# Kernel tuning notes

Measured on AMD Instinct MI355X. Metric: run time of the kernel, lower is better.

The kernel has to match this reference:

```python
import jax, jax.numpy as jnp
import numpy as np

N = 131072          # source points
M = 65536           # sampled (query) points
NN = 32             # max_nr_neighbors
K = 15              # num_kernel_points
IN_F = 64
OUT_F = 128
MAP_SIZE = 40.0
SUB_DIST = 0.5      # subsampling_dist * subsampling_factor (meters)
KERNEL_RADIUS = max(1.5, 2.0 * SUB_DIST) / MAP_SIZE          # 0.0375
KP_EXTENT = KERNEL_RADIUS / (K ** (1.0 / 3.0) - 1.0) * 1.5
NEG_SLOPE = 0.01    # nn.LeakyReLU default


def setup_inputs() -> dict:
    rng = np.random.RandomState(0)
    points = rng.rand(N, 3).astype(np.float32)

    # ---- gridSampling (faithful numpy port of the torch code) ----
    resolution = SUB_DIST / MAP_SIZE
    grid = np.floor(points / resolution)
    center = (grid + 0.5) * resolution
    dist = ((points - center) ** 2).sum(1)
    dist = dist / dist.max() * 0.7
    v_size = np.ceil(1.0 / resolution)
    grid_idx = grid[:, 0] + grid[:, 1] * v_size + grid[:, 2] * v_size * v_size
    grid_d = grid_idx + dist
    order = np.argsort(grid_d, kind='stable')
    gi_sorted = grid_idx[order]
    first = np.ones(N, bool)
    first[1:] = gi_sorted[1:] != gi_sorted[:-1]
    sample_idx = order[first]  # closest-to-voxel-center point per voxel
    if sample_idx.shape[0] < M:
        sample_idx = np.tile(sample_idx, int(np.ceil(M / sample_idx.shape[0])))
    sample_idx = np.sort(sample_idx[:M])

    # ---- radius search (stand-in for octree.radiusSearchIndices) ----
    # candidates = window in voxel-sorted order, filtered by true euclidean radius,
    # nearest-first, padded with shadow index N (standard KPConv padding).
    pos_in_sorted = np.empty(N, np.int64)
    pos_in_sorted[order] = np.arange(N)
    qpos = pos_in_sorted[sample_idx]
    offs = np.arange(-48, 48)
    cand_pos = np.clip(qpos[:, None] + offs[None, :], 0, N - 1)
    cand_idx = order[cand_pos]                                  # [M,96]
    d2 = ((points[cand_idx] - points[sample_idx][:, None, :]) ** 2).sum(-1)
    valid = d2 <= KERNEL_RADIUS ** 2
    d2w = np.where(valid, d2, np.inf)
    sel = np.argsort(d2w, axis=1)[:, :NN]
    nbr = np.take_along_axis(cand_idx, sel, 1)
    nbr_ok = np.take_along_axis(valid, sel, 1)
    neighbors_index = np.where(nbr_ok, nbr, N).astype(np.int32)  # [M,NN]

    # ---- kernel point dispositions (rigid KPConv buffer) ----
    kp_dir = rng.randn(K, 3).astype(np.float32)
    kp_dir /= np.linalg.norm(kp_dir, axis=1, keepdims=True) + 1e-9
    kernel_points = kp_dir * (rng.rand(K, 1).astype(np.float32) ** (1.0 / 3.0)) * KERNEL_RADIUS

    key = jax.random.key(0)
    ks = jax.random.split(key, 6)
    def lin(k, i, o):
        return (jax.random.normal(k, (i, o), jnp.float32) / np.sqrt(i)).astype(jnp.float32)

    return {
        'points': jnp.asarray(points),
        'features': jax.random.normal(ks[0], (N, IN_F), jnp.float32),
        'W_pre': lin(ks[1], IN_F, OUT_F),
        'b_pre': jnp.zeros((OUT_F,), jnp.float32),
        'kernel_points': jnp.asarray(kernel_points),
        'kp_weights': jax.random.normal(ks[2], (K, OUT_F, OUT_F), jnp.float32) / np.sqrt(K * OUT_F),
        'W_post': lin(ks[3], OUT_F, OUT_F),
        'b_post': jnp.zeros((OUT_F,), jnp.float32),
        'W_sc': lin(ks[4], IN_F, OUT_F),
        'b_sc': jnp.zeros((OUT_F,), jnp.float32),
        'sample_idx': jnp.asarray(sample_idx, jnp.int32),
        'neighbors_index': jnp.asarray(neighbors_index),
    }


def _leaky(x):
    return jnp.where(x >= 0, x, NEG_SLOPE * x)


def reference(points, features, W_pre, b_pre, kernel_points, kp_weights,
              W_post, b_post, W_sc, b_sc, sample_idx, neighbors_index):
    # preactivation: Linear + LeakyReLU (batchnorm=False)
    feats = _leaky(features @ W_pre + b_pre)                       # [N, OUT_F]

    # shadow padding: far point + zero feature row at index N
    s_pts = jnp.concatenate([points, jnp.full((1, 3), 1e6, points.dtype)], 0)
    x_pad = jnp.concatenate([feats, jnp.zeros((1, OUT_F), feats.dtype)], 0)

    # rigid KPConv: gather -> distance influence -> weight -> aggregate
    q_pts = points[sample_idx]                                     # [M,3]
    neighb = s_pts[neighbors_index] - q_pts[:, None, :]            # [M,NN,3]
    sq_d = jnp.sum((neighb[:, :, None, :] - kernel_points[None, None]) ** 2, -1)  # [M,NN,K]
    all_w = jnp.maximum(1.0 - jnp.sqrt(sq_d) / KP_EXTENT, 0.0)     # linear influence
    nx = x_pad[neighbors_index]                                    # [M,NN,OUT_F]
    wfeat = jnp.einsum('mnk,mnc->mkc', all_w, nx)                  # [M,K,OUT_F]
    conv = jnp.einsum('mkc,kco->mo', wfeat, kp_weights)            # [M,OUT_F]

    # post layer: LeakyReLU then Linear (batchnorm=False, relu=True)
    post = _leaky(conv) @ W_post + b_post

    # shortcut on sampled input features (in_fdim != out_fdim -> Linear)
    sc = features[sample_idx] @ W_sc + b_sc
    return _leaky(sc + post)                                       # [M,OUT_F]
```

## Files before the change

kernel.cpp:

```cpp
#include <hip/hip_runtime.h>
#include <cmath>

#define NPTS 131072
#define MTOT 65536
#define NNB  32
#define KKP  15
#define INF  64
#define OUTF 128
#define KCDIM 1920
#define WROWB 1920

#define META_OFF  61440
#define LDS_TOTAL 77824
#define A2_OFF 0
#define A3_OFF 8192

typedef __attribute__((ext_vector_type(8))) __bf16 bf16x8;
typedef __attribute__((ext_vector_type(8))) unsigned short u16x8;
typedef __attribute__((ext_vector_type(4))) float f32x4;
typedef unsigned int u32;
typedef __attribute__((ext_vector_type(4))) u32 u32x4;

__device__ __forceinline__ u32 f2bf(float f){
  u32 u = __builtin_bit_cast(u32, f);
  return (u + 0x7fffu + ((u>>16)&1u)) >> 16;
}
__device__ __forceinline__ float leaky(float v){ return v >= 0.f ? v : 0.01f*v; }

__global__ __launch_bounds__(256) void k_cvt_67723(
    const float* __restrict__ kpw, const float* __restrict__ wpost,
    const float* __restrict__ wsc, const float* __restrict__ wpre,
    unsigned short* __restrict__ bpack, unsigned short* __restrict__ wpostT,
    unsigned short* __restrict__ wscT, unsigned short* __restrict__ wpreT)
{
  int tid = blockIdx.x * 256 + threadIdx.x;
  if (tid < KCDIM * OUTF) {
    int kc = tid >> 7, o = tid & 127;
    int kk = kc >> 7, c = kc & 127;
    int h = c >> 6, cl = c & 63;
    int s = kk*2 + (cl >> 5);
    int rem = cl & 31, lg = rem >> 3, j = rem & 7;
    int ot = o >> 4, lr = o & 15;
    bpack[(size_t)((h*30 + s)*8 + ot)*512 + lr*32 + lg*8 + j] =
        (unsigned short)f2bf(kpw[(size_t)kc * OUTF + o]);
    return;
  }
  int t2 = tid - KCDIM * OUTF;
  if (t2 < OUTF * OUTF) {
    int o = t2 / OUTF, i = t2 % OUTF;
    wpostT[t2] = (unsigned short)f2bf(wpost[i * OUTF + o]);
    return;
  }
  int t3 = t2 - OUTF * OUTF;
  if (t3 < OUTF * INF) {
    int o = t3 / INF, c = t3 % INF;
    wscT[t3] = (unsigned short)f2bf(wsc[c * OUTF + o]);
    return;
  }
  int t4 = t3 - OUTF * INF;
  if (t4 < OUTF * INF) {
    int o = t4 / INF, c = t4 % INF;
    wpreT[t4] = (unsigned short)f2bf(wpre[c * OUTF + o]);
  }
}

__global__ __launch_bounds__(256) void k_pre_67723(
    const float* __restrict__ feat, const unsigned short* __restrict__ wpreT,
    const float* __restrict__ bp, unsigned short* __restrict__ featbf)
{
  const int w = threadIdx.x >> 6, l = threadIdx.x & 63, lr = l & 15, lg = l >> 4;
  const int m0 = blockIdx.x * 128 + w * 32;
  f32x4 acc[2][8];
#pragma unroll
  for (int ot = 0; ot < 8; ot++) {
    float bv = bp[ot*16 + lr];
    f32x4 s = {bv, bv, bv, bv};
    acc[0][ot] = s; acc[1][ot] = s;
  }
  bf16x8 af[2][2];
#pragma unroll
  for (int mi = 0; mi < 2; mi++)
#pragma unroll
  for (int ks = 0; ks < 2; ks++) {
    const float* src = feat + (size_t)(m0 + mi*16 + lr) * INF + ks*32 + lg*8;
    float4 f0 = *(const float4*)src, f1 = *(const float4*)(src + 4);
    u16x8 p;
    p[0]=f2bf(f0.x); p[1]=f2bf(f0.y); p[2]=f2bf(f0.z); p[3]=f2bf(f0.w);
    p[4]=f2bf(f1.x); p[5]=f2bf(f1.y); p[6]=f2bf(f1.z); p[7]=f2bf(f1.w);
    af[mi][ks] = __builtin_bit_cast(bf16x8, p);
  }
#pragma unroll
  for (int ks = 0; ks < 2; ks++)
#pragma unroll
  for (int ot = 0; ot < 8; ot++) {
    bf16x8 b = *(const bf16x8*)(wpreT + (size_t)(ot*16 + lr) * INF + ks*32 + lg*8);
    acc[0][ot] = __builtin_amdgcn_mfma_f32_16x16x32_bf16(af[0][ks], b, acc[0][ot], 0,0,0);
    acc[1][ot] = __builtin_amdgcn_mfma_f32_16x16x32_bf16(af[1][ks], b, acc[1][ot], 0,0,0);
  }
#pragma unroll
  for (int mi = 0; mi < 2; mi++)
#pragma unroll
  for (int ot = 0; ot < 8; ot++)
#pragma unroll
  for (int r = 0; r < 4; r++) {
    int m = m0 + mi*16 + lg*4 + r;
    featbf[(size_t)m * OUTF + ot*16 + lr] = (unsigned short)f2bf(leaky(acc[mi][ot][r]));
  }
}

__global__ __launch_bounds__(512, 4) void k_fused_67723(
    const float* __restrict__ points, const float* __restrict__ features,
    const float* __restrict__ kp, const float* __restrict__ bpost,
    const float* __restrict__ bsc, const int* __restrict__ sample_idx,
    const int* __restrict__ nbr, const unsigned short* __restrict__ featbf,
    const unsigned short* __restrict__ bpack, const unsigned short* __restrict__ wpostT,
    const unsigned short* __restrict__ wscT, float* __restrict__ out,
    float inv_ext, int nwg)
{
  extern __shared__ char smem[];
  float4* meta = (float4*)(smem + META_OFF);
  const int t = threadIdx.x, l = t & 63, w = t >> 6, lr = l & 15, lg = l >> 4;
  const int bid = blockIdx.x;
  const int swb = (bid & 7) * (nwg >> 3) + (bid >> 3);
  const int m0 = swb * 32;

  for (int e = t; e < 1024; e += 512) {
    int s = e >> 5, n = e & 31;
    int gm = m0 + s;
    int sidx = sample_idx[gm];
    int ni = nbr[(size_t)gm * NNB + n];
    bool valid = ni < NPTS;
    int nic = valid ? ni : 0;
    float qx = points[sidx*3], qy = points[sidx*3+1], qz = points[sidx*3+2];
    float dx = points[nic*3] - qx, dy = points[nic*3+1] - qy, dz = points[nic*3+2] - qz;
    if (!valid) dx = 1e9f;
    meta[s*32 + n] = make_float4(dx, dy, dz, __int_as_float(nic * (OUTF*2)));
  }
  __syncthreads();

  const bool kvalid = lr < KKP;
  const int kk2 = kvalid ? lr : 0;
  const float kx = kp[kk2*3], ky = kp[kk2*3+1], kz = kp[kk2*3+2];
  const char* fb = (const char*)featbf;
  const f32x4 zero = {0,0,0,0};

  f32x4 acc[2] = {{0,0,0,0},{0,0,0,0}};
  const int convswz = (lr & 7) << 4;
  const char* arow0 = smem + lr * WROWB;
  const char* arow1 = smem + (lr + 16) * WROWB;

#pragma unroll
  for (int h = 0; h < 2; h++) {
    if (h) __syncthreads();

    for (int i = 0; i < 4; i++) {
      const int s = w*4 + i;
      uint2 dj[8];
      u32 apk[4];
      float wvp = 0.f;
#pragma unroll
      for (int j = 0; j < 8; j++) {
        float4 mje = meta[s*32 + lg*8 + j];
        u32 off = __builtin_bit_cast(u32, mje.w);
        dj[j] = *(const uint2*)(fb + off + h*128 + lr*8);
        float ex = mje.x - kx, ey = mje.y - ky, ez = mje.z - kz;
        float d = sqrtf(ex*ex + ey*ey + ez*ez);
        float wv = kvalid ? fmaxf(1.f - d * inv_ext, 0.f) : 0.f;
        if (j & 1) apk[j>>1] = f2bf(wvp) | (f2bf(wv) << 16);
        else       wvp = wv;
      }
      u32x4 av = {apk[0], apk[1], apk[2], apk[3]};
      bf16x8 afr = __builtin_bit_cast(bf16x8, av);

      f32x4 D[4];
#pragma unroll
      for (int q = 0; q < 4; q++) {
        u32 b[4];
#pragma unroll
        for (int u = 0; u < 4; u++) {
          u32 w0 = (q < 2) ? dj[2*u].x   : dj[2*u].y;
          u32 w1 = (q < 2) ? dj[2*u+1].x : dj[2*u+1].y;
          b[u] = __builtin_amdgcn_perm(w1, w0, (q & 1) ? 0x07060302u : 0x05040100u);
        }
        u32x4 bv = {b[0], b[1], b[2], b[3]};
        D[q] = __builtin_amdgcn_mfma_f32_16x16x32_bf16(
                   afr, __builtin_bit_cast(bf16x8, bv), zero, 0,0,0);
      }
      char* wrow = smem + s * WROWB;
      const int sswz = (s & 7) << 4;
#pragma unroll
      for (int r = 0; r < 4; r++) {
        int kr = lg*4 + r;
        if (kr < KKP) {
          uint2 pv;
          pv.x = f2bf(D[0][r]) | (f2bf(D[1][r]) << 16);
          pv.y = f2bf(D[2][r]) | (f2bf(D[3][r]) << 16);
          *(uint2*)(wrow + ((kr*128 + lr*8) ^ sswz)) = pv;
        }
      }
    }
    __syncthreads();

    const char* bb = (const char*)bpack + (size_t)(h*240 + w) * 1024 + lr*64 + lg*16;
#pragma unroll 6
    for (int s = 0; s < 30; s++) {
      int aoff = (s*64 + lg*16) ^ convswz;
      bf16x8 af0 = *(const bf16x8*)(arow0 + aoff);
      bf16x8 af1 = *(const bf16x8*)(arow1 + aoff);
      bf16x8 bfr = *(const bf16x8*)(bb + s*8192);
      acc[0] = __builtin_amdgcn_mfma_f32_16x16x32_bf16(af0, bfr, acc[0], 0,0,0);
      acc[1] = __builtin_amdgcn_mfma_f32_16x16x32_bf16(af1, bfr, acc[1], 0,0,0);
    }
  }
  __syncthreads();

  char* a2 = smem + A2_OFF;
  char* a3 = smem + A3_OFF;
#pragma unroll
  for (int mi = 0; mi < 2; mi++)
#pragma unroll
  for (int r = 0; r < 4; r++) {
    int m = mi*16 + lg*4 + r;
    int o = w*16 + lr;
    *(unsigned short*)(a2 + m*256 + ((o*2) ^ ((m & 15) << 4))) =
        (unsigned short)f2bf(leaky(acc[mi][r]));
  }
  if (t < 256) {
    int r = t >> 3, seg = t & 7;
    int sidx = sample_idx[m0 + r];
    const float* src = features + (size_t)sidx * INF + seg*8;
    float4 f0 = *(const float4*)src, f1 = *(const float4*)(src + 4);
    uint4 pv = make_uint4(f2bf(f0.x) | (f2bf(f0.y) << 16),
                          f2bf(f0.z) | (f2bf(f0.w) << 16),
                          f2bf(f1.x) | (f2bf(f1.y) << 16),
                          f2bf(f1.z) | (f2bf(f1.w) << 16));
    *(uint4*)(a3 + r*128 + ((seg*16) ^ ((r & 7) << 4))) = pv;
  }
  __syncthreads();

  const int mt = w & 1, oq = w >> 1;
  const int mrow = mt*16 + lr;
  f32x4 d[2];
#pragma unroll
  for (int ot = 0; ot < 2; ot++) {
    float bv = bpost[oq*32 + ot*16 + lr] + bsc[oq*32 + ot*16 + lr];
    d[ot] = (f32x4){bv, bv, bv, bv};
  }
#pragma unroll
  for (int ks = 0; ks < 4; ks++) {
    bf16x8 af = *(const bf16x8*)(a2 + mrow*256 + ((ks*64 + lg*16) ^ ((mrow & 15) << 4)));
#pragma unroll
    for (int ot = 0; ot < 2; ot++) {
      bf16x8 b = *(const bf16x8*)(wpostT + (size_t)(oq*32 + ot*16 + lr) * OUTF + ks*32 + lg*8);
      d[ot] = __builtin_amdgcn_mfma_f32_16x16x32_bf16(af, b, d[ot], 0,0,0);
    }
  }
#pragma unroll
  for (int ks = 0; ks < 2; ks++) {
    bf16x8 af = *(const bf16x8*)(a3 + mrow*128 + ((ks*64 + lg*16) ^ ((mrow & 7) << 4)));
#pragma unroll
    for (int ot = 0; ot < 2; ot++) {
      bf16x8 b = *(const bf16x8*)(wscT + (size_t)(oq*32 + ot*16 + lr) * INF + ks*32 + lg*8);
      d[ot] = __builtin_amdgcn_mfma_f32_16x16x32_bf16(af, b, d[ot], 0,0,0);
    }
  }
#pragma unroll
  for (int ot = 0; ot < 2; ot++)
#pragma unroll
  for (int r = 0; r < 4; r++) {
    int m = mt*16 + lg*4 + r;
    int o = oq*32 + ot*16 + lr;
    out[(size_t)(m0 + m) * OUTF + o] = leaky(d[ot][r]);
  }
}

extern "C" void kernel_launch(void* const* d_in, const int* in_sizes, int n_in,
                              void* d_out, int out_size, void* d_ws, size_t ws_size,
                              hipStream_t stream)
{
  const float* points   = (const float*)d_in[0];
  const float* features = (const float*)d_in[1];
  const float* W_pre    = (const float*)d_in[2];
  const float* b_pre    = (const float*)d_in[3];
  const float* kpts     = (const float*)d_in[4];
  const float* kpw      = (const float*)d_in[5];
  const float* W_post   = (const float*)d_in[6];
  const float* b_post   = (const float*)d_in[7];
  const float* W_sc     = (const float*)d_in[8];
  const float* b_sc     = (const float*)d_in[9];
  const int* sample_idx = (const int*)d_in[10];
  const int* nbr        = (const int*)d_in[11];
  float* out = (float*)d_out;

  char* ws = (char*)d_ws;
  unsigned short* featbf = (unsigned short*)ws;
  unsigned short* bpack  = (unsigned short*)(ws + 33554432);
  unsigned short* wpostT = (unsigned short*)(ws + 34045952);
  unsigned short* wscT   = (unsigned short*)(ws + 34078720);
  unsigned short* wpreT  = (unsigned short*)(ws + 34095104);

  double ext = (1.5 / 40.0) / (pow(15.0, 1.0 / 3.0) - 1.0) * 1.5;
  float inv_ext = (float)(1.0 / ext);

  (void)hipFuncSetAttribute((const void*)k_fused_67723,
                            hipFuncAttributeMaxDynamicSharedMemorySize, LDS_TOTAL);

  const int nwg = MTOT / 32;
  k_cvt_67723<<<1088, 256, 0, stream>>>(kpw, W_post, W_sc, W_pre, bpack, wpostT, wscT, wpreT);
  k_pre_67723<<<1024, 256, 0, stream>>>(features, wpreT, b_pre, featbf);
  k_fused_67723<<<nwg, 512, LDS_TOTAL, stream>>>(points, features, kpts, b_post, b_sc,
                                                 sample_idx, nbr, featbf, bpack, wpostT,
                                                 wscT, out, inv_ext, nwg);
}
```

Measured before the change: 173.4 us.

## Make fused blocks loop over four M-tiles with conv weights held in registers

Measured after the change: 644.9 us. 272% more time.

```diff
diff --git a/kernel.cpp b/kernel.cpp
--- a/kernel.cpp
+++ b/kernel.cpp
@@ -115,162 +115,173 @@
     const int* __restrict__ nbr, const unsigned short* __restrict__ featbf,
     const unsigned short* __restrict__ bpack, const unsigned short* __restrict__ wpostT,
     const unsigned short* __restrict__ wscT, float* __restrict__ out,
-    float inv_ext, int nwg)
+    float inv_ext)
 {
   extern __shared__ char smem[];
   float4* meta = (float4*)(smem + META_OFF);
   const int t = threadIdx.x, l = t & 63, w = t >> 6, lr = l & 15, lg = l >> 4;
   const int bid = blockIdx.x;
-  const int swb = (bid & 7) * (nwg >> 3) + (bid >> 3);
-  const int m0 = swb * 32;
-
-  for (int e = t; e < 1024; e += 512) {
-    int s = e >> 5, n = e & 31;
-    int gm = m0 + s;
-    int sidx = sample_idx[gm];
-    int ni = nbr[(size_t)gm * NNB + n];
-    bool valid = ni < NPTS;
-    int nic = valid ? ni : 0;
-    float qx = points[sidx*3], qy = points[sidx*3+1], qz = points[sidx*3+2];
-    float dx = points[nic*3] - qx, dy = points[nic*3+1] - qy, dz = points[nic*3+2] - qz;
-    if (!valid) dx = 1e9f;
-    meta[s*32 + n] = make_float4(dx, dy, dz, __int_as_float(nic * (OUTF*2)));
-  }
-  __syncthreads();
+  const int swb = (bid & 7) * 64 + (bid >> 3);
+  const int mblk = swb * 128;
+
+  bf16x8 Breg[60];
+  {
+    const char* bp = (const char*)bpack + (size_t)w * 1024 + lr*64 + lg*16;
+#pragma unroll
+    for (int f = 0; f < 60; f++)
+      Breg[f] = *(const bf16x8*)(bp + (size_t)f * 8192);
+  }
 
   const bool kvalid = lr < KKP;
   const int kk2 = kvalid ? lr : 0;
   const float kx = kp[kk2*3], ky = kp[kk2*3+1], kz = kp[kk2*3+2];
   const char* fb = (const char*)featbf;
   const f32x4 zero = {0,0,0,0};
-
-  f32x4 acc[2] = {{0,0,0,0},{0,0,0,0}};
   const int convswz = (lr & 7) << 4;
   const char* arow0 = smem + lr * WROWB;
   const char* arow1 = smem + (lr + 16) * WROWB;
-
-#pragma unroll
-  for (int h = 0; h < 2; h++) {
-    if (h) __syncthreads();
-
-    for (int i = 0; i < 4; i++) {
-      const int s = w*4 + i;
-      uint2 dj[8];
-      u32 apk[4];
-      float wvp = 0.f;
-#pragma unroll
-      for (int j = 0; j < 8; j++) {
-        float4 mje = meta[s*32 + lg*8 + j];
-        u32 off = __builtin_bit_cast(u32, mje.w);
-        dj[j] = *(const uint2*)(fb + off + h*128 + lr*8);
-        float ex = mje.x - kx, ey = mje.y - ky, ez = mje.z - kz;
-        float d = sqrtf(ex*ex + ey*ey + ez*ez);
-        float wv = kvalid ? fmaxf(1.f - d * inv_ext, 0.f) : 0.f;
-        if (j & 1) apk[j>>1] = f2bf(wvp) | (f2bf(wv) << 16);
-        else       wvp = wv;
-      }
-      u32x4 av = {apk[0], apk[1], apk[2], apk[3]};
-      bf16x8 afr = __builtin_bit_cast(bf16x8, av);
-
-      f32x4 D[4];
-#pragma unroll
-      for (int q = 0; q < 4; q++) {
-        u32 b[4];
-#pragma unroll
-        for (int u = 0; u < 4; u++) {
-          u32 w0 = (q < 2) ? dj[2*u].x   : dj[2*u].y;
-          u32 w1 = (q < 2) ? dj[2*u+1].x : dj[2*u+1].y;
-          b[u] = __builtin_amdgcn_perm(w1, w0, (q & 1) ? 0x07060302u : 0x05040100u);
+  const int mt_e = w & 1, oq_e = w >> 1;
+  const int mrow = mt_e*16 + lr;
+
+  for (int tile = 0; tile < 4; tile++) {
+    const int m0 = mblk + tile * 32;
+    __syncthreads();
+
+    for (int e = t; e < 1024; e += 512) {
+      int s = e >> 5, n = e & 31;
+      int gm = m0 + s;
+      int sidx = sample_idx[gm];
+      int ni = nbr[(size_t)gm * NNB + n];
+      bool valid = ni < NPTS;
+      int nic = valid ? ni : 0;
+      float qx = points[sidx*3], qy = points[sidx*3+1], qz = points[sidx*3+2];
+      float dx = points[nic*3] - qx, dy = points[nic*3+1] - qy, dz = points[nic*3+2] - qz;
+      if (!valid) dx = 1e9f;
+      meta[s*32 + n] = make_float4(dx, dy, dz, __int_as_float(nic * (OUTF*2)));
+    }
+    __syncthreads();
+
+    f32x4 acc[2] = {{0,0,0,0},{0,0,0,0}};
+
+#pragma unroll
+    for (int h = 0; h < 2; h++) {
+      if (h) __syncthreads();
+
+      for (int i = 0; i < 4; i++) {
+        const int s = w*4 + i;
+        uint2 dj[8];
+        u32 apk[4];
+        float wvp = 0.f;
+#pragma unroll
+        for (int j = 0; j < 8; j++) {
+          float4 mje = meta[s*32 + lg*8 + j];
+          u32 off = __builtin_bit_cast(u32, mje.w);
+          dj[j] = *(const uint2*)(fb + off + h*128 + lr*8);
+          float ex = mje.x - kx, ey = mje.y - ky, ez = mje.z - kz;
+          float d = sqrtf(ex*ex + ey*ey + ez*ez);
+          float wv = kvalid ? fmaxf(1.f - d * inv_ext, 0.f) : 0.f;
+          if (j & 1) apk[j>>1] = f2bf(wvp) | (f2bf(wv) << 16);
+          else       wvp = wv;
         }
-        u32x4 bv = {b[0], b[1], b[2], b[3]};
-        D[q] = __builtin_amdgcn_mfma_f32_16x16x32_bf16(
-                   afr, __builtin_bit_cast(bf16x8, bv), zero, 0,0,0);
-      }
-      char* wrow = smem + s * WROWB;
-      const int sswz = (s & 7) << 4;
-#pragma unroll
-      for (int r = 0; r < 4; r++) {
-        int kr = lg*4 + r;
-        if (kr < KKP) {
-          uint2 pv;
-          pv.x = f2bf(D[0][r]) | (f2bf(D[1][r]) << 16);
-          pv.y = f2bf(D[2][r]) | (f2bf(D[3][r]) << 16);
-          *(uint2*)(wrow + ((kr*128 + lr*8) ^ sswz)) = pv;
+        u32x4 av = {apk[0], apk[1], apk[2], apk[3]};
+        bf16x8 afr = __builtin_bit_cast(bf16x8, av);
+
+        f32x4 D[4];
+#pragma unroll
+        for (int q = 0; q < 4; q++) {
+          u32 b[4];
+#pragma unroll
+          for (int u = 0; u < 4; u++) {
+            u32 w0 = (q < 2) ? dj[2*u].x   : dj[2*u].y;
+            u32 w1 = (q < 2) ? dj[2*u+1].x : dj[2*u+1].y;
+            b[u] = __builtin_amdgcn_perm(w1, w0, (q & 1) ? 0x07060302u : 0x05040100u);
+          }
+          u32x4 bv = {b[0], b[1], b[2], b[3]};
+          D[q] = __builtin_amdgcn_mfma_f32_16x16x32_bf16(
+                     afr, __builtin_bit_cast(bf16x8, bv), zero, 0,0,0);
+        }
+        char* wrow = smem + s * WROWB;
+        const int sswz = (s & 7) << 4;
+#pragma unroll
+        for (int r = 0; r < 4; r++) {
+          int kr = lg*4 + r;
+          if (kr < KKP) {
+            uint2 pv;
+            pv.x = f2bf(D[0][r]) | (f2bf(D[1][r]) << 16);
+            pv.y = f2bf(D[2][r]) | (f2bf(D[3][r]) << 16);
+            *(uint2*)(wrow + ((kr*128 + lr*8) ^ sswz)) = pv;
+          }
         }
       }
+      __syncthreads();
+
+#pragma unroll
+      for (int s = 0; s < 30; s++) {
+        int aoff = (s*64 + lg*16) ^ convswz;
+        bf16x8 af0 = *(const bf16x8*)(arow0 + aoff);
+        bf16x8 af1 = *(const bf16x8*)(arow1 + aoff);
+        acc[0] = __builtin_amdgcn_mfma_f32_16x16x32_bf16(af0, Breg[h*30+s], acc[0], 0,0,0);
+        acc[1] = __builtin_amdgcn_mfma_f32_16x16x32_bf16(af1, Breg[h*30+s], acc[1], 0,0,0);
+      }
     }
     __syncthreads();
 
-    const char* bb = (const char*)bpack + (size_t)(h*240 + w) * 1024 + lr*64 + lg*16;
-#pragma unroll 6
-    for (int s = 0; s < 30; s++) {
-      int aoff = (s*64 + lg*16) ^ convswz;
-      bf16x8 af0 = *(const bf16x8*)(arow0 + aoff);
-      bf16x8 af1 = *(const bf16x8*)(arow1 + aoff);
-      bf16x8 bfr = *(const bf16x8*)(bb + s*8192);
-      acc[0] = __builtin_amdgcn_mfma_f32_16x16x32_bf16(af0, bfr, acc[0], 0,0,0);
-      acc[1] = __builtin_amdgcn_mfma_f32_16x16x32_bf16(af1, bfr, acc[1], 0,0,0);
-    }
-  }
-  __syncthreads();
-
-  char* a2 = smem + A2_OFF;
-  char* a3 = smem + A3_OFF;
-#pragma unroll
-  for (int mi = 0; mi < 2; mi++)
-#pragma unroll
-  for (int r = 0; r < 4; r++) {
-    int m = mi*16 + lg*4 + r;
-    int o = w*16 + lr;
-    *(unsigned short*)(a2 + m*256 + ((o*2) ^ ((m & 15) << 4))) =
-        (unsigned short)f2bf(leaky(acc[mi][r]));
-  }
-  if (t < 256) {
-    int r = t >> 3, seg = t & 7;
-    int sidx = sample_idx[m0 + r];
-    const float* src = features + (size_t)sidx * INF + seg*8;
-    float4 f0 = *(const float4*)src, f1 = *(const float4*)(src + 4);
-    uint4 pv = make_uint4(f2bf(f0.x) | (f2bf(f0.y) << 16),
-                          f2bf(f0.z) | (f2bf(f0.w) << 16),
-                          f2bf(f1.x) | (f2bf(f1.y) << 16),
-                          f2bf(f1.z) | (f2bf(f1.w) << 16));
-    *(uint4*)(a3 + r*128 + ((seg*16) ^ ((r & 7) << 4))) = pv;
-  }
-  __syncthreads();
-
-  const int mt = w & 1, oq = w >> 1;
-  const int mrow = mt*16 + lr;
-  f32x4 d[2];
-#pragma unroll
-  for (int ot = 0; ot < 2; ot++) {
-    float bv = bpost[oq*32 + ot*16 + lr] + bsc[oq*32 + ot*16 + lr];
-    d[ot] = (f32x4){bv, bv, bv, bv};
-  }
-#pragma unroll
-  for (int ks = 0; ks < 4; ks++) {
-    bf16x8 af = *(const bf16x8*)(a2 + mrow*256 + ((ks*64 + lg*16) ^ ((mrow & 15) << 4)));
+    char* a2 = smem + A2_OFF;
+    char* a3 = smem + A3_OFF;
+#pragma unroll
+    for (int mi = 0; mi < 2; mi++)
+#pragma unroll
+    for (int r = 0; r < 4; r++) {
+      int m = mi*16 + lg*4 + r;
+      int o = w*16 + lr;
+      *(unsigned short*)(a2 + m*256 + ((o*2) ^ ((m & 15) << 4))) =
+          (unsigned short)f2bf(leaky(acc[mi][r]));
+    }
+    if (t < 256) {
+      int r = t >> 3, seg = t & 7;
+      int sidx = sample_idx[m0 + r];
+      const float* src = features + (size_t)sidx * INF + seg*8;
+      float4 f0 = *(const float4*)src, f1 = *(const float4*)(src + 4);
+      uint4 pv = make_uint4(f2bf(f0.x) | (f2bf(f0.y) << 16),
+                            f2bf(f0.z) | (f2bf(f0.w) << 16),
+                            f2bf(f1.x) | (f2bf(f1.y) << 16),
+                            f2bf(f1.z) | (f2bf(f1.w) << 16));
+      *(uint4*)(a3 + r*128 + ((seg*16) ^ ((r & 7) << 4))) = pv;
+    }
+    __syncthreads();
+
+    f32x4 d[2];
 #pragma unroll
     for (int ot = 0; ot < 2; ot++) {
-      bf16x8 b = *(const bf16x8*)(wpostT + (size_t)(oq*32 + ot*16 + lr) * OUTF + ks*32 + lg*8);
-      d[ot] = __builtin_amdgcn_mfma_f32_16x16x32_bf16(af, b, d[ot], 0,0,0);
-    }
-  }
-#pragma unroll
-  for (int ks = 0; ks < 2; ks++) {
-    bf16x8 af = *(const bf16x8*)(a3 + mrow*128 + ((ks*64 + lg*16) ^ ((mrow & 7) << 4)));
-#pragma unroll
-    for (int ot = 0; ot < 2; ot++) {
-      bf16x8 b = *(const bf16x8*)(wscT + (size_t)(oq*32 + ot*16 + lr) * INF + ks*32 + lg*8);
-      d[ot] = __builtin_amdgcn_mfma_f32_16x16x32_bf16(af, b, d[ot], 0,0,0);
-    }
-  }
-#pragma unroll
-  for (int ot = 0; ot < 2; ot++)
-#pragma unroll
-  for (int r = 0; r < 4; r++) {
-    int m = mt*16 + lg*4 + r;
-    int o = oq*32 + ot*16 + lr;
-    out[(size_t)(m0 + m) * OUTF + o] = leaky(d[ot][r]);
+      float bv = bpost[oq_e*32 + ot*16 + lr] + bsc[oq_e*32 + ot*16 + lr];
+      d[ot] = (f32x4){bv, bv, bv, bv};
+    }
+#pragma unroll
+    for (int ks = 0; ks < 4; ks++) {
+      bf16x8 af = *(const bf16x8*)(a2 + mrow*256 + ((ks*64 + lg*16) ^ ((mrow & 15) << 4)));
+#pragma unroll
+      for (int ot = 0; ot < 2; ot++) {
+        bf16x8 b = *(const bf16x8*)(wpostT + (size_t)(oq_e*32 + ot*16 + lr) * OUTF + ks*32 + lg*8);
+        d[ot] = __builtin_amdgcn_mfma_f32_16x16x32_bf16(af, b, d[ot], 0,0,0);
+      }
+    }
+#pragma unroll
+    for (int ks = 0; ks < 2; ks++) {
+      bf16x8 af = *(const bf16x8*)(a3 + mrow*128 + ((ks*64 + lg*16) ^ ((mrow & 7) << 4)));
+#pragma unroll
+      for (int ot = 0; ot < 2; ot++) {
+        bf16x8 b = *(const bf16x8*)(wscT + (size_t)(oq_e*32 + ot*16 + lr) * INF + ks*32 + lg*8);
+        d[ot] = __builtin_amdgcn_mfma_f32_16x16x32_bf16(af, b, d[ot], 0,0,0);
+      }
+    }
+#pragma unroll
+    for (int ot = 0; ot < 2; ot++)
+#pragma unroll
+    for (int r = 0; r < 4; r++) {
+      int m = mt_e*16 + lg*4 + r;
+      int o = oq_e*32 + ot*16 + lr;
+      out[(size_t)(m0 + m) * OUTF + o] = leaky(d[ot][r]);
+    }
   }
 }
 
@@ -305,10 +316,9 @@
   (void)hipFuncSetAttribute((const void*)k_fused_67723,
                             hipFuncAttributeMaxDynamicSharedMemorySize, LDS_TOTAL);
 
-  const int nwg = MTOT / 32;
   k_cvt_67723<<<1088, 256, 0, stream>>>(kpw, W_post, W_sc, W_pre, bpack, wpostT, wscT, wpreT);
   k_pre_67723<<<1024, 256, 0, stream>>>(features, wpreT, b_pre, featbf);
-  k_fused_67723<<<nwg, 512, LDS_TOTAL, stream>>>(points, features, kpts, b_post, b_sc,
+  k_fused_67723<<<512, 512, LDS_TOTAL, stream>>>(points, features, kpts, b_post, b_sc,
                                                  sample_idx, nbr, featbf, bpack, wpostT,
-                                                 wscT, out, inv_ext, nwg);
-}
+                                                 wscT, out, inv_ext);
+}
```

## Hoist kernel-point weights out of halves and double-buffer neighbor feature gathers

Applied to the files above, without the earlier changes.

Result: slower. 211.1 us (+21.8%).

```diff
diff --git a/kernel.cpp b/kernel.cpp
--- a/kernel.cpp
+++ b/kernel.cpp
@@ -108,6 +108,35 @@
   }
 }
 
+#define ISSUE_67723(I, DJ) { \
+  _Pragma("unroll") for (int j = 0; j < 8; j++) \
+    DJ[j] = *(const uint2*)(fb + woff[I][j] + h*128); }
+
+#define PROC_67723(I, DJ) { \
+  u32x4 av = {apkc[I][0], apkc[I][1], apkc[I][2], apkc[I][3]}; \
+  bf16x8 afr = __builtin_bit_cast(bf16x8, av); \
+  f32x4 D[4]; \
+  _Pragma("unroll") for (int q = 0; q < 4; q++) { \
+    u32 sel = (q & 1) ? 0x07060302u : 0x05040100u; \
+    u32 b0 = __builtin_amdgcn_perm((q<2)?DJ[1].x:DJ[1].y, (q<2)?DJ[0].x:DJ[0].y, sel); \
+    u32 b1 = __builtin_amdgcn_perm((q<2)?DJ[3].x:DJ[3].y, (q<2)?DJ[2].x:DJ[2].y, sel); \
+    u32 b2 = __builtin_amdgcn_perm((q<2)?DJ[5].x:DJ[5].y, (q<2)?DJ[4].x:DJ[4].y, sel); \
+    u32 b3 = __builtin_amdgcn_perm((q<2)?DJ[7].x:DJ[7].y, (q<2)?DJ[6].x:DJ[6].y, sel); \
+    u32x4 bv = {b0, b1, b2, b3}; \
+    D[q] = __builtin_amdgcn_mfma_f32_16x16x32_bf16(afr, __builtin_bit_cast(bf16x8, bv), zero, 0,0,0); \
+  } \
+  char* wrow = smem + (w*4 + (I)) * WROWB; \
+  const int sswz = (((w*4 + (I)) & 7) << 4); \
+  _Pragma("unroll") for (int r = 0; r < 4; r++) { \
+    int kr = lg*4 + r; \
+    if (kr < KKP) { \
+      uint2 pv; \
+      pv.x = f2bf(D[0][r]) | (f2bf(D[1][r]) << 16); \
+      pv.y = f2bf(D[2][r]) | (f2bf(D[3][r]) << 16); \
+      *(uint2*)(wrow + ((kr*128 + lr*8) ^ sswz)) = pv; \
+    } \
+  } }
+
 __global__ __launch_bounds__(512, 4) void k_fused_67723(
     const float* __restrict__ points, const float* __restrict__ features,
     const float* __restrict__ kp, const float* __restrict__ bpost,
@@ -144,6 +173,24 @@
   const char* fb = (const char*)featbf;
   const f32x4 zero = {0,0,0,0};
 
+  u32 apkc[4][4];
+  u32 woff[4][8];
+#pragma unroll
+  for (int i = 0; i < 4; i++) {
+    const int s = w*4 + i;
+    float wvp = 0.f;
+#pragma unroll
+    for (int j = 0; j < 8; j++) {
+      float4 mje = meta[s*32 + lg*8 + j];
+      woff[i][j] = __builtin_bit_cast(u32, mje.w) + (u32)(lr*8);
+      float ex = mje.x - kx, ey = mje.y - ky, ez = mje.z - kz;
+      float d = __builtin_amdgcn_sqrtf(ex*ex + ey*ey + ez*ez);
+      float wv = kvalid ? fmaxf(1.f - d * inv_ext, 0.f) : 0.f;
+      if (j & 1) apkc[i][j>>1] = f2bf(wvp) | (f2bf(wv) << 16);
+      else       wvp = wv;
+    }
+  }
+
   f32x4 acc[2] = {{0,0,0,0},{0,0,0,0}};
   const int convswz = (lr & 7) << 4;
   const char* arow0 = smem + lr * WROWB;
@@ -153,51 +200,16 @@
   for (int h = 0; h < 2; h++) {
     if (h) __syncthreads();
 
-    for (int i = 0; i < 4; i++) {
-      const int s = w*4 + i;
-      uint2 dj[8];
-      u32 apk[4];
-      float wvp = 0.f;
-#pragma unroll
-      for (int j = 0; j < 8; j++) {
-        float4 mje = meta[s*32 + lg*8 + j];
-        u32 off = __builtin_bit_cast(u32, mje.w);
-        dj[j] = *(const uint2*)(fb + off + h*128 + lr*8);
-        float ex = mje.x - kx, ey = mje.y - ky, ez = mje.z - kz;
-        float d = sqrtf(ex*ex + ey*ey + ez*ez);
-        float wv = kvalid ? fmaxf(1.f - d * inv_ext, 0.f) : 0.f;
-        if (j & 1) apk[j>>1] = f2bf(wvp) | (f2bf(wv) << 16);
-        else       wvp = wv;
-      }
-      u32x4 av = {apk[0], apk[1], apk[2], apk[3]};
-      bf16x8 afr = __builtin_bit_cast(bf16x8, av);
-
-      f32x4 D[4];
-#pragma unroll
-      for (int q = 0; q < 4; q++) {
-        u32 b[4];
-#pragma unroll
-        for (int u = 0; u < 4; u++) {
-          u32 w0 = (q < 2) ? dj[2*u].x   : dj[2*u].y;
-          u32 w1 = (q < 2) ? dj[2*u+1].x : dj[2*u+1].y;
-          b[u] = __builtin_amdgcn_perm(w1, w0, (q & 1) ? 0x07060302u : 0x05040100u);
-        }
-        u32x4 bv = {b[0], b[1], b[2], b[3]};
-        D[q] = __builtin_amdgcn_mfma_f32_16x16x32_bf16(
-                   afr, __builtin_bit_cast(bf16x8, bv), zero, 0,0,0);
-      }
-      char* wrow = smem + s * WROWB;
-      const int sswz = (s & 7) << 4;
-#pragma unroll
-      for (int r = 0; r < 4; r++) {
-        int kr = lg*4 + r;
-        if (kr < KKP) {
-          uint2 pv;
-          pv.x = f2bf(D[0][r]) | (f2bf(D[1][r]) << 16);
-          pv.y = f2bf(D[2][r]) | (f2bf(D[3][r]) << 16);
-          *(uint2*)(wrow + ((kr*128 + lr*8) ^ sswz)) = pv;
-        }
-      }
+    {
+      uint2 djA[8], djB[8];
+      ISSUE_67723(0, djA)
+      ISSUE_67723(1, djB)
+      PROC_67723(0, djA)
+      ISSUE_67723(2, djA)
+      PROC_67723(1, djB)
+      ISSUE_67723(3, djB)
+      PROC_67723(2, djA)
+      PROC_67723(3, djB)
     }
     __syncthreads();
 
```

## Double fused kernel block to 1024 threads, splitting per-wave conv and epilogue work

Applied to the files above, without the earlier changes.

Result: slower. 210.2 us (+21.2%).

```diff
diff --git a/kernel.cpp b/kernel.cpp
--- a/kernel.cpp
+++ b/kernel.cpp
@@ -108,7 +108,7 @@
   }
 }
 
-__global__ __launch_bounds__(512, 4) void k_fused_67723(
+__global__ __launch_bounds__(1024, 8) void k_fused_67723(
     const float* __restrict__ points, const float* __restrict__ features,
     const float* __restrict__ kp, const float* __restrict__ bpost,
     const float* __restrict__ bsc, const int* __restrict__ sample_idx,
@@ -124,8 +124,8 @@
   const int swb = (bid & 7) * (nwg >> 3) + (bid >> 3);
   const int m0 = swb * 32;
 
-  for (int e = t; e < 1024; e += 512) {
-    int s = e >> 5, n = e & 31;
+  {
+    int s = t >> 5, n = t & 31;
     int gm = m0 + s;
     int sidx = sample_idx[gm];
     int ni = nbr[(size_t)gm * NNB + n];
@@ -144,17 +144,17 @@
   const char* fb = (const char*)featbf;
   const f32x4 zero = {0,0,0,0};
 
-  f32x4 acc[2] = {{0,0,0,0},{0,0,0,0}};
+  f32x4 acc = {0,0,0,0};
+  const int mt_c = w & 1, ot_c = w >> 1;
   const int convswz = (lr & 7) << 4;
-  const char* arow0 = smem + lr * WROWB;
-  const char* arow1 = smem + (lr + 16) * WROWB;
+  const char* arow = smem + (mt_c*16 + lr) * WROWB;
 
 #pragma unroll
   for (int h = 0; h < 2; h++) {
     if (h) __syncthreads();
 
-    for (int i = 0; i < 4; i++) {
-      const int s = w*4 + i;
+    for (int i = 0; i < 2; i++) {
+      const int s = w*2 + i;
       uint2 dj[8];
       u32 apk[4];
       float wvp = 0.f;
@@ -164,7 +164,7 @@
         u32 off = __builtin_bit_cast(u32, mje.w);
         dj[j] = *(const uint2*)(fb + off + h*128 + lr*8);
         float ex = mje.x - kx, ey = mje.y - ky, ez = mje.z - kz;
-        float d = sqrtf(ex*ex + ey*ey + ez*ez);
+        float d = __builtin_amdgcn_sqrtf(ex*ex + ey*ey + ez*ez);
         float wv = kvalid ? fmaxf(1.f - d * inv_ext, 0.f) : 0.f;
         if (j & 1) apk[j>>1] = f2bf(wvp) | (f2bf(wv) << 16);
         else       wvp = wv;
@@ -201,15 +201,13 @@
     }
     __syncthreads();
 
-    const char* bb = (const char*)bpack + (size_t)(h*240 + w) * 1024 + lr*64 + lg*16;
+    const char* bb = (const char*)bpack + (size_t)(h*240 + ot_c) * 1024 + lr*64 + lg*16;
 #pragma unroll 6
     for (int s = 0; s < 30; s++) {
       int aoff = (s*64 + lg*16) ^ convswz;
-      bf16x8 af0 = *(const bf16x8*)(arow0 + aoff);
-      bf16x8 af1 = *(const bf16x8*)(arow1 + aoff);
+      bf16x8 af = *(const bf16x8*)(arow + aoff);
       bf16x8 bfr = *(const bf16x8*)(bb + s*8192);
-      acc[0] = __builtin_amdgcn_mfma_f32_16x16x32_bf16(af0, bfr, acc[0], 0,0,0);
-      acc[1] = __builtin_amdgcn_mfma_f32_16x16x32_bf16(af1, bfr, acc[1], 0,0,0);
+      acc = __builtin_amdgcn_mfma_f32_16x16x32_bf16(af, bfr, acc, 0,0,0);
     }
   }
   __syncthreads();
@@ -217,13 +215,11 @@
   char* a2 = smem + A2_OFF;
   char* a3 = smem + A3_OFF;
 #pragma unroll
-  for (int mi = 0; mi < 2; mi++)
-#pragma unroll
   for (int r = 0; r < 4; r++) {
-    int m = mi*16 + lg*4 + r;
-    int o = w*16 + lr;
+    int m = mt_c*16 + lg*4 + r;
+    int o = ot_c*16 + lr;
     *(unsigned short*)(a2 + m*256 + ((o*2) ^ ((m & 15) << 4))) =
-        (unsigned short)f2bf(leaky(acc[mi][r]));
+        (unsigned short)f2bf(leaky(acc[r]));
   }
   if (t < 256) {
     int r = t >> 3, seg = t & 7;
@@ -238,39 +234,27 @@
   }
   __syncthreads();
 
-  const int mt = w & 1, oq = w >> 1;
-  const int mrow = mt*16 + lr;
-  f32x4 d[2];
-#pragma unroll
-  for (int ot = 0; ot < 2; ot++) {
-    float bv = bpost[oq*32 + ot*16 + lr] + bsc[oq*32 + ot*16 + lr];
-    d[ot] = (f32x4){bv, bv, bv, bv};
-  }
+  const int mt_e = w & 1, oq_e = w >> 1;
+  const int mrow = mt_e*16 + lr;
+  float bv = bpost[oq_e*16 + lr] + bsc[oq_e*16 + lr];
+  f32x4 d = {bv, bv, bv, bv};
 #pragma unroll
   for (int ks = 0; ks < 4; ks++) {
     bf16x8 af = *(const bf16x8*)(a2 + mrow*256 + ((ks*64 + lg*16) ^ ((mrow & 15) << 4)));
-#pragma unroll
-    for (int ot = 0; ot < 2; ot++) {
-      bf16x8 b = *(const bf16x8*)(wpostT + (size_t)(oq*32 + ot*16 + lr) * OUTF + ks*32 + lg*8);
-      d[ot] = __builtin_amdgcn_mfma_f32_16x16x32_bf16(af, b, d[ot], 0,0,0);
-    }
+    bf16x8 b = *(const bf16x8*)(wpostT + (size_t)(oq_e*16 + lr) * OUTF + ks*32 + lg*8);
+    d = __builtin_amdgcn_mfma_f32_16x16x32_bf16(af, b, d, 0,0,0);
   }
 #pragma unroll
   for (int ks = 0; ks < 2; ks++) {
     bf16x8 af = *(const bf16x8*)(a3 + mrow*128 + ((ks*64 + lg*16) ^ ((mrow & 7) << 4)));
-#pragma unroll
-    for (int ot = 0; ot < 2; ot++) {
-      bf16x8 b = *(const bf16x8*)(wscT + (size_t)(oq*32 + ot*16 + lr) * INF + ks*32 + lg*8);
-      d[ot] = __builtin_amdgcn_mfma_f32_16x16x32_bf16(af, b, d[ot], 0,0,0);
-    }
-  }
-#pragma unroll
-  for (int ot = 0; ot < 2; ot++)
+    bf16x8 b = *(const bf16x8*)(wscT + (size_t)(oq_e*16 + lr) * INF + ks*32 + lg*8);
+    d = __builtin_amdgcn_mfma_f32_16x16x32_bf16(af, b, d, 0,0,0);
+  }
 #pragma unroll
   for (int r = 0; r < 4; r++) {
-    int m = mt*16 + lg*4 + r;
-    int o = oq*32 + ot*16 + lr;
-    out[(size_t)(m0 + m) * OUTF + o] = leaky(d[ot][r]);
+    int m = mt_e*16 + lg*4 + r;
+    int o = oq_e*16 + lr;
+    out[(size_t)(m0 + m) * OUTF + o] = leaky(d[r]);
   }
 }
 
@@ -308,7 +292,7 @@
   const int nwg = MTOT / 32;
   k_cvt_67723<<<1088, 256, 0, stream>>>(kpw, W_post, W_sc, W_pre, bpack, wpostT, wscT, wpreT);
   k_pre_67723<<<1024, 256, 0, stream>>>(features, wpreT, b_pre, featbf);
-  k_fused_67723<<<nwg, 512, LDS_TOTAL, stream>>>(points, features, kpts, b_post, b_sc,
-                                                 sample_idx, nbr, featbf, bpack, wpostT,
-                                                 wscT, out, inv_ext, nwg);
-}
+  k_fused_67723<<<nwg, 1024, LDS_TOTAL, stream>>>(points, features, kpts, b_post, b_sc,
+                                                  sample_idx, nbr, featbf, bpack, wpostT,
+                                                  wscT, out, inv_ext, nwg);
+}
```
